# Kernel tuning notes

Hardware: AMD Instinct MI355X
Metric: run time of the kernel (lower is better)

## Reference

```python
import jax, jax.numpy as jnp
import numpy as np

# Static architecture sizes (see shape_source)
B, H, W, NCH = 64, 64, 64, 3
K = 2                     # kernel at every stage
D = 20                    # bond_dim == virtual_dim
OUT = 10                  # output_dim
P1 = (H // K) * (W // K)          # 1024 patches, stage 1
P2 = P1 // (K * K)                # 256 patches, stage 2
P3 = P2 // (K * K)                # 64 patches, stage 3
FP = 2 * K * K                    # feature_dim per stage = 2*ker^2 = 8
FF = 2 * D                        # feature_dim of final MPS = 2*virtual_dim


def _unfold(x, k):
    # torch: x.unfold(2,k,k).unfold(3,k,k).reshape(b, k*k, -1, C)
    b, C, Hh, Ww = x.shape
    v = x.reshape(b, C, Hh // k, k, Ww // k, k).transpose(0, 1, 2, 4, 3, 5)
    return v.reshape(b, k * k, -1, C)   # [b, k^2, P, C] (raw reshape, faithful)


def _batchnorm(y, g, bb, eps=1e-5):
    # BatchNorm1d(C) on [b, C, L], training mode (batch stats), affine
    mu = jnp.mean(y, axis=(0, 2), keepdims=True)
    var = jnp.var(y, axis=(0, 2), keepdims=True)
    return g[None, :, None] * (y - mu) * jax.lax.rsqrt(var + eps) + bb[None, :, None]


def _mps(x, cores, label, alpha, omega):
    # Batched tensor-train contraction over independent per-patch MPS modules.
    # x:     [b, Fraw, P, S]  (S sites per MPS, P independent MPS modules)
    # cores: [P, S, 2*Fraw, D, D], label: [O, D, D], alpha/omega: [D]
    phi = jnp.concatenate([x, 1.0 - x], axis=1)              # [b, F, P, S]
    M = jnp.einsum('bfps,psfij->spbij', phi, cores)          # per-site transfer mats
    def step(c, m):
        return jnp.einsum('pbij,pbjk->pbik', c, m), None
    eye = jnp.broadcast_to(jnp.eye(cores.shape[-1], dtype=x.dtype), M.shape[1:])
    tot, _ = jax.lax.scan(step, eye, M)                      # [P, b, D, D]
    return jnp.einsum('i,pbij,ojk,k->bpo', alpha, tot, label, omega)  # [b, P, O]


def _cores(key, P, S, F):
    # near-identity init; sum_f phi_f = Fraw = F/2, so scale eye by 2/F
    return (jnp.eye(D, dtype=jnp.float32) * (2.0 / F)
            + 0.01 * jax.random.normal(key, (P, S, F, D, D), jnp.float32))


def setup_inputs() -> dict:
    ks = jax.random.split(jax.random.key(0), 12)
    one, zero = jnp.ones((D,), jnp.float32), jnp.zeros
    return {
        'x': jax.random.normal(ks[0], (B, NCH, H, W), jnp.float32),
        'cores1': _cores(ks[1], P1, NCH, FP),
        'label1': 0.1 * jax.random.normal(ks[2], (D, D, D), jnp.float32),
        'alpha1': one, 'omega1': one,
        'g1': jnp.ones((P1,), jnp.float32), 'b1': zero((P1,), jnp.float32),
        'cores2': _cores(ks[3], P2, D, FP),
        'label2': 0.1 * jax.random.normal(ks[4], (D, D, D), jnp.float32),
        'alpha2': one, 'omega2': one,
        'g2': jnp.ones((P2,), jnp.float32), 'b2': zero((P2,), jnp.float32),
        'cores3': _cores(ks[5], P3, D, FP),
        'label3': 0.1 * jax.random.normal(ks[6], (D, D, D), jnp.float32),
        'alpha3': one, 'omega3': one,
        'g3': jnp.ones((P3,), jnp.float32), 'b3': zero((P3,), jnp.float32),
        'coresF': _cores(ks[7], 1, P3, FF),
        'labelF': 0.1 * jax.random.normal(ks[8], (OUT, D, D), jnp.float32),
        'alphaF': one, 'omegaF': one,
    }


def reference(x, cores1, label1, alpha1, omega1, g1, b1,
              cores2, label2, alpha2, omega2, g2, b2,
              cores3, label3, alpha3, omega3, g3, b3,
              coresF, labelF, alphaF, omegaF):
    b = x.shape[0]
    u = _unfold(x, K)                              # [b, 4, P1, 3]
    y = _mps(u, cores1, label1, alpha1, omega1)    # [b, P1, D]
    y = _batchnorm(y, g1, b1).reshape(b, D, H // K, W // K)   # raw view, faithful
    u = _unfold(y, K)                              # [b, 4, P2, D]
    y = _mps(u, cores2, label2, alpha2, omega2)    # [b, P2, D]
    y = _batchnorm(y, g2, b2).reshape(b, D, H // (K * K), W // (K * K))
    u = _unfold(y, K)                              # [b, 4, P3, D]
    y = _mps(u, cores3, label3, alpha3, omega3)    # [b, P3, D]
    y = _batchnorm(y, g3, b3)
    y = jnp.transpose(y, (0, 2, 1))                # [b, D, P3]
    out = _mps(y[:, :, None, :], coresF, labelF, alphaF, omegaF)[:, 0, :]
    return out                                     # [b, OUT]
```

## Files before the change

### kernel.cpp

```cpp
#include <hip/hip_runtime.h>
#include <hip/hip_bf16.h>

typedef __attribute__((ext_vector_type(4))) float f32x4;
typedef __attribute__((ext_vector_type(8))) short s16x8;

static __device__ __forceinline__ short f2bf(float x) {
  __hip_bfloat16 h = __float2bfloat16(x);
  return *reinterpret_cast<short*>(&h);
}

static __device__ __forceinline__ void wave_lgkm0() {
  asm volatile("s_waitcnt lgkmcnt(0)" ::: "memory");
  __builtin_amdgcn_sched_barrier(0);
}

template<int STAGE>
__global__ __launch_bounds__(256)
void k_mps(const float* __restrict__ xsrc, const float* __restrict__ ysrc,
           const float* __restrict__ cores, const float* __restrict__ alpha,
           const float* __restrict__ label, const float* __restrict__ omega,
           const float* __restrict__ gam, const float* __restrict__ bet,
           float* __restrict__ yout) {
  constexpr int S = (STAGE == 1) ? 3 : 20;
  __shared__ __align__(16) float u4[S][64][4];
  __shared__ __align__(16) short Cl[2][32][168];
  __shared__ __align__(16) float vls[64][36];
  __shared__ float Lw_l[400];
  __shared__ float redA[4], redB[4], stats[2];

  const int p = blockIdx.x, t = threadIdx.x;
  const int b = t & 63, q = t >> 6;
  const int m = b & 15, quad = b >> 4;
  const int bl = q * 16 + m;

  const bool two = (t < 144);
  const float* cbase = cores + (size_t)p * S * 3200;

  float p0A[8], p0B[8], p1A[8], p1B[8];
#pragma unroll
  for (int g = 0; g < 8; ++g) p0A[g] = cbase[g * 400 + t];
  if (two) {
#pragma unroll
    for (int g = 0; g < 8; ++g) p0B[g] = cbase[g * 400 + 256 + t];
  }

  for (int e = t; e < 400; e += 256) {
    int o = e / 20, j = e % 20;
    float a = 0.f;
#pragma unroll
    for (int k = 0; k < 20; ++k) a = fmaf(label[o * 400 + j * 20 + k], omega[k], a);
    Lw_l[e] = a;
  }

  {
    int* cz = (int*)&Cl[0][0][0];
    for (int i = t; i < 5376; i += 256) cz[i] = 0;
    for (int i = t; i < 64 * 36; i += 256) {
      int col = i % 36;
      vls[i / 36][col] = (col < 20) ? alpha[col] : 0.f;
    }
  }

  float vr0[4], vr1[4];
  {
    float a0 = alpha[m];
    float a1 = (m < 4) ? alpha[m + 16] : 0.f;
#pragma unroll
    for (int r = 0; r < 4; ++r) { vr0[r] = a0; vr1[r] = a1; }
  }

  for (int k = 0; k < S; ++k) {
    float val;
    if (STAGE == 1) {
      int L = q * 3072 + p * 3 + k;
      int c = L >> 12, r = L & 4095;
      int hh = 2 * (r >> 7) + ((r >> 1) & 1);
      int ww = 2 * ((r >> 2) & 31) + (r & 1);
      val = xsrc[(b * 3 + c) * 4096 + hh * 64 + ww];
    } else if (STAGE == 2) {
      int L = q * 5120 + p * 20 + k;
      int c = L >> 10, r = L & 1023;
      int f = c * 1024 + (2 * (r >> 6) + ((r >> 1) & 1)) * 32
                        + (2 * ((r >> 2) & 15) + (r & 1));
      val = ysrc[f * 64 + b];
    } else {
      int L = q * 1280 + p * 20 + k;
      int c = L >> 8, r = L & 255;
      int f = c * 256 + (2 * (r >> 5) + ((r >> 1) & 1)) * 16
                       + (2 * ((r >> 2) & 7) + (r & 1));
      val = ysrc[f * 64 + b];
    }
    u4[k][b][q] = val;
  }

  auto writeC = [&](int buf, int e, const float* r) {
    int i = e / 20, j = e % 20;
    Cl[buf][j][      i] = f2bf(r[0] - r[4]);
    Cl[buf][j][ 32 + i] = f2bf(r[1] - r[5]);
    Cl[buf][j][ 64 + i] = f2bf(r[2] - r[6]);
    Cl[buf][j][ 96 + i] = f2bf(r[3] - r[7]);
    float cs = r[4] + r[5] + r[6] + r[7];
    if (i == j) cs -= 1.f;
    Cl[buf][j][128 + i] = f2bf(cs);
  };
  auto loadSite = [&](int s, float (&rA)[8], float (&rB)[8]) {
    const float* cs = cbase + (size_t)s * 3200;
#pragma unroll
    for (int g = 0; g < 8; ++g) rA[g] = cs[g * 400 + t];
    if (two) {
#pragma unroll
      for (int g = 0; g < 8; ++g) rB[g] = cs[g * 400 + 256 + t];
    }
  };

  writeC(0, t, p0A);
  if (two) writeC(0, t + 256, p0B);
  if (S > 1) loadSite(1, p0A, p0B);
  if (S > 2) loadSite(2, p1A, p1B);
  __syncthreads();

  auto site_step = [&](int s, int cur, float (&rA)[8], float (&rB)[8]) {
    const float4 uu = *(const float4*)&u4[s][bl][0];
    const float4 va = *(const float4*)&vls[bl][quad * 8];
    const float4 vb = *(const float4*)&vls[bl][quad * 8 + 4];
    const float vv[8] = {va.x, va.y, va.z, va.w, vb.x, vb.y, vb.z, vb.w};
    const float um[5] = {uu.x, uu.y, uu.z, uu.w, 1.f};

    f32x4 acc0, acc1;
#pragma unroll
    for (int r = 0; r < 4; ++r) { acc0[r] = vr0[r]; acc1[r] = vr1[r]; }
#pragma unroll
    for (int kt = 0; kt < 5; ++kt) {
      s16x8 aF;
#pragma unroll
      for (int j2 = 0; j2 < 8; ++j2) aF[j2] = f2bf(vv[j2] * um[kt]);
      const s16x8 bF0 = *(const s16x8*)&Cl[cur][m][kt * 32 + quad * 8];
      const s16x8 bF1 = *(const s16x8*)&Cl[cur][m + 16][kt * 32 + quad * 8];
      acc0 = __builtin_amdgcn_mfma_f32_16x16x32_bf16(aF, bF0, acc0, 0, 0, 0);
      acc1 = __builtin_amdgcn_mfma_f32_16x16x32_bf16(aF, bF1, acc1, 0, 0, 0);
    }

    if (s + 1 < S) {
      writeC(cur ^ 1, t, rA);
      if (two) writeC(cur ^ 1, t + 256, rB);
      if (s + 3 < S) loadSite(s + 3, rA, rB);
    }

#pragma unroll
    for (int r = 0; r < 4; ++r) { vr0[r] = acc0[r]; vr1[r] = acc1[r]; }
#pragma unroll
    for (int r = 0; r < 4; ++r) vls[q * 16 + quad * 4 + r][m] = acc0[r];
    if (m < 4) {
#pragma unroll
      for (int r = 0; r < 4; ++r) vls[q * 16 + quad * 4 + r][m + 16] = acc1[r];
    }
    __syncthreads();
  };

  for (int s = 0; s < S; s += 2) {
    site_step(s, 0, p0A, p0B);
    if (s + 1 < S) site_step(s + 1, 1, p1A, p1B);
  }

  float vf[20];
  {
    const float4 v0 = *(const float4*)&vls[b][0];
    const float4 v1 = *(const float4*)&vls[b][4];
    const float4 v2 = *(const float4*)&vls[b][8];
    const float4 v3 = *(const float4*)&vls[b][12];
    const float4 v4 = *(const float4*)&vls[b][16];
    vf[0]=v0.x; vf[1]=v0.y; vf[2]=v0.z; vf[3]=v0.w;
    vf[4]=v1.x; vf[5]=v1.y; vf[6]=v1.z; vf[7]=v1.w;
    vf[8]=v2.x; vf[9]=v2.y; vf[10]=v2.z; vf[11]=v2.w;
    vf[12]=v3.x; vf[13]=v3.y; vf[14]=v3.z; vf[15]=v3.w;
    vf[16]=v4.x; vf[17]=v4.y; vf[18]=v4.z; vf[19]=v4.w;
  }
  float yo[5];
  float s1 = 0.f, s2 = 0.f;
#pragma unroll
  for (int jj = 0; jj < 5; ++jj) {
    int o = q * 5 + jj;
    float a = 0.f;
#pragma unroll
    for (int j = 0; j < 20; ++j) a = fmaf(vf[j], Lw_l[o * 20 + j], a);
    yo[jj] = a; s1 += a; s2 += a * a;
  }
#pragma unroll
  for (int off = 32; off > 0; off >>= 1) {
    s1 += __shfl_down(s1, off); s2 += __shfl_down(s2, off);
  }
  if (b == 0) { redA[q] = s1; redB[q] = s2; }
  __syncthreads();
  if (t == 0) {
    float S1 = redA[0] + redA[1] + redA[2] + redA[3];
    float S2 = redB[0] + redB[1] + redB[2] + redB[3];
    float mu = S1 * (1.f / 1280.f);
    float var = S2 * (1.f / 1280.f) - mu * mu;
    if (var < 0.f) var = 0.f;
    stats[0] = mu; stats[1] = var;
  }
  __syncthreads();
  float mu = stats[0], var = stats[1];
  float scale = gam[p] / sqrtf(var + 1e-5f);
  float shift = bet[p] - mu * scale;
#pragma unroll
  for (int jj = 0; jj < 5; ++jj) {
    int o = q * 5 + jj;
    yout[(p * 20 + o) * 64 + b] = fmaf(yo[jj], scale, shift);
  }
}

__global__ __launch_bounds__(256)
void k_mbuild(const float* __restrict__ yn3, const float* __restrict__ coresF,
              float* __restrict__ Mmat) {
  __shared__ float ybn[64][20];
  const int s = blockIdx.x >> 2, bq = blockIdx.x & 3;
  const int t = threadIdx.x;
  for (int i = t; i < 1280; i += 256) ybn[i & 63][i >> 6] = yn3[(size_t)s * 1280 + i];
  __syncthreads();
  const float* cfp = coresF + (size_t)s * 16000;
  for (int e = t; e < 400; e += 256) {
    float dlt[20]; float hsum = 0.f;
#pragma unroll
    for (int g = 0; g < 20; ++g) {
      float lo = cfp[g * 400 + e], hi = cfp[(g + 20) * 400 + e];
      dlt[g] = lo - hi; hsum += hi;
    }
    for (int bb = bq * 16; bb < bq * 16 + 16; ++bb) {
      const float4* yb = (const float4*)ybn[bb];
      float yy[20];
      *(float4*)&yy[0]  = yb[0]; *(float4*)&yy[4]  = yb[1];
      *(float4*)&yy[8]  = yb[2]; *(float4*)&yy[12] = yb[3];
      *(float4*)&yy[16] = yb[4];
      float a = hsum;
#pragma unroll
      for (int g = 0; g < 20; ++g) a = fmaf(yy[g], dlt[g], a);
      Mmat[((size_t)s * 64 + bb) * 400 + e] = a;
    }
  }
}

__global__ __launch_bounds__(512)
void k_fin(const float* __restrict__ Mmat, const float* __restrict__ alphaF,
           const float* __restrict__ labelF, const float* __restrict__ omegaF,
           float* __restrict__ out) {
  const int bb = blockIdx.x, t = threadIdx.x;
  const int w = t >> 6, l = t & 63;
  __shared__ float Pw[8][2][400];
  __shared__ float Mw[8][400];
  __shared__ float chunkP[8][400];
  __shared__ float LwF[200];
  __shared__ float va[20];

  if (t < 200) {
    int o = t / 20, j = t % 20;
    float a = 0.f;
#pragma unroll
    for (int k = 0; k < 20; ++k) a = fmaf(labelF[o * 400 + j * 20 + k], omegaF[k], a);
    LwF[t] = a;
  }

  float pre[7];
  {
    const size_t b0 = ((size_t)(w * 8) * 64 + bb) * 400;
#pragma unroll
    for (int it = 0; it < 7; ++it) {
      int e = l + 64 * it;
      pre[it] = (e < 400) ? Mmat[b0 + e] : 0.f;
    }
#pragma unroll
    for (int it = 0; it < 7; ++it) {
      int e = l + 64 * it;
      if (e < 400) Pw[w][0][e] = pre[it];
    }
  }
  int cur = 0;
  for (int ls = 1; ls < 8; ++ls) {
    const size_t mb = ((size_t)(w * 8 + ls) * 64 + bb) * 400;
#pragma unroll
    for (int it = 0; it < 7; ++it) {
      int e = l + 64 * it;
      if (e < 400) pre[it] = Mmat[mb + e];
    }
#pragma unroll
    for (int it = 0; it < 7; ++it) {
      int e = l + 64 * it;
      if (e < 400) Mw[w][e] = pre[it];
    }
    wave_lgkm0();
    if (l < 60) {
      const int j = l % 20, ii = l / 20;
      float mc[20];
#pragma unroll
      for (int k = 0; k < 20; ++k) mc[k] = Mw[w][k * 20 + j];
      for (int i = ii; i < 20; i += 3) {
        float a = 0.f;
#pragma unroll
        for (int k = 0; k < 20; ++k) a = fmaf(Pw[w][cur][i * 20 + k], mc[k], a);
        Pw[w][cur ^ 1][i * 20 + j] = a;
      }
    }
    wave_lgkm0();
    cur ^= 1;
  }
#pragma unroll
  for (int it = 0; it < 7; ++it) {
    int e = l + 64 * it;
    if (e < 400) chunkP[w][e] = Pw[w][cur][e];
  }
  __syncthreads();

  float* T0 = &Mw[0][0];
  float* T1 = &Mw[1][0];
  if (t < 400) T0[t] = chunkP[0][t];
  __syncthreads();
  float* Tc = T0; float* Tn = T1;
  for (int c = 1; c < 8; ++c) {
    if (t < 400) {
      int i = t / 20, j = t - (t / 20) * 20;
      float a = 0.f;
#pragma unroll
      for (int k = 0; k < 20; ++k) a = fmaf(Tc[i * 20 + k], chunkP[c][k * 20 + j], a);
      Tn[t] = a;
    }
    __syncthreads();
    float* tmp = Tc; Tc = Tn; Tn = tmp;
  }
  if (t < 20) {
    float a = 0.f;
#pragma unroll
    for (int i = 0; i < 20; ++i) a = fmaf(alphaF[i], Tc[i * 20 + t], a);
    va[t] = a;
  }
  __syncthreads();
  if (t < 10) {
    float a = 0.f;
#pragma unroll
    for (int j = 0; j < 20; ++j) a = fmaf(va[j], LwF[t * 20 + j], a);
    out[bb * 10 + t] = a;
  }
}

extern "C" void kernel_launch(void* const* d_in, const int* in_sizes, int n_in,
                              void* d_out, int out_size, void* d_ws, size_t ws_size,
                              hipStream_t stream) {
  const float* x      = (const float*)d_in[0];
  const float* cores1 = (const float*)d_in[1];
  const float* label1 = (const float*)d_in[2];
  const float* alpha1 = (const float*)d_in[3];
  const float* omega1 = (const float*)d_in[4];
  const float* g1     = (const float*)d_in[5];
  const float* b1     = (const float*)d_in[6];
  const float* cores2 = (const float*)d_in[7];
  const float* label2 = (const float*)d_in[8];
  const float* alpha2 = (const float*)d_in[9];
  const float* omega2 = (const float*)d_in[10];
  const float* g2     = (const float*)d_in[11];
  const float* b2     = (const float*)d_in[12];
  const float* cores3 = (const float*)d_in[13];
  const float* label3 = (const float*)d_in[14];
  const float* alpha3 = (const float*)d_in[15];
  const float* omega3 = (const float*)d_in[16];
  const float* g3     = (const float*)d_in[17];
  const float* b3     = (const float*)d_in[18];
  const float* coresF = (const float*)d_in[19];
  const float* labelF = (const float*)d_in[20];
  const float* alphaF = (const float*)d_in[21];
  const float* omegaF = (const float*)d_in[22];

  float* ws   = (float*)d_ws;
  float* yn1  = ws;
  float* yn2  = yn1 + 1310720;
  float* yn3  = yn2 + 327680;
  float* Mmat = yn3 + 81920;
  float* out  = (float*)d_out;

  k_mps<1><<<1024, 256, 0, stream>>>(x, nullptr, cores1, alpha1, label1, omega1, g1, b1, yn1);
  k_mps<2><<<256, 256, 0, stream>>>(nullptr, yn1, cores2, alpha2, label2, omega2, g2, b2, yn2);
  k_mps<3><<<64, 256, 0, stream>>>(nullptr, yn2, cores3, alpha3, label3, omega3, g3, b3, yn3);
  k_mbuild<<<256, 256, 0, stream>>>(yn3, coresF, Mmat);
  k_fin<<<64, 512, 0, stream>>>(Mmat, alphaF, labelF, omegaF, out);
}
```

Before: 254.2 us.

## Fuse final-MPS matrix build into stage 3 and split chain product across blocks

Stage 3 now writes its batch-normalised output to shared memory and builds the final MPS transfer matrices directly, which removes the separate k_mbuild launch and the yn3 round trip. The final chain product, previously 64 blocks of 512 threads, is split into 512 single-wave blocks that each multiply 8 matrices with register prefetch and float4 LDS reads, followed by a small kernel that combines the 8 chunk products per batch element. This raises parallelism in the sequential tail in exchange for an extra launch and a global chunk buffer. The fused stage-3 matrix build runs on only 64 blocks, each looping over all 64 batch entries, so it may itself become slower.

```diff
diff --git a/kernel.cpp b/kernel.cpp
--- a/kernel.cpp
+++ b/kernel.cpp
@@ -20,7 +20,8 @@
            const float* __restrict__ cores, const float* __restrict__ alpha,
            const float* __restrict__ label, const float* __restrict__ omega,
            const float* __restrict__ gam, const float* __restrict__ bet,
-           float* __restrict__ yout) {
+           float* __restrict__ yout, const float* __restrict__ coresF,
+           float* __restrict__ Mmat) {
   constexpr int S = (STAGE == 1) ? 3 : 20;
   __shared__ __align__(16) float u4[S][64][4];
   __shared__ __align__(16) short Cl[2][32][168];
@@ -203,101 +204,105 @@
   float mu = stats[0], var = stats[1];
   float scale = gam[p] / sqrtf(var + 1e-5f);
   float shift = bet[p] - mu * scale;
-#pragma unroll
-  for (int jj = 0; jj < 5; ++jj) {
-    int o = q * 5 + jj;
-    yout[(p * 20 + o) * 64 + b] = fmaf(yo[jj], scale, shift);
-  }
-}
-
-__global__ __launch_bounds__(256)
-void k_mbuild(const float* __restrict__ yn3, const float* __restrict__ coresF,
-              float* __restrict__ Mmat) {
-  __shared__ float ybn[64][20];
-  const int s = blockIdx.x >> 2, bq = blockIdx.x & 3;
-  const int t = threadIdx.x;
-  for (int i = t; i < 1280; i += 256) ybn[i & 63][i >> 6] = yn3[(size_t)s * 1280 + i];
-  __syncthreads();
-  const float* cfp = coresF + (size_t)s * 16000;
-  for (int e = t; e < 400; e += 256) {
-    float dlt[20]; float hsum = 0.f;
-#pragma unroll
-    for (int g = 0; g < 20; ++g) {
-      float lo = cfp[g * 400 + e], hi = cfp[(g + 20) * 400 + e];
-      dlt[g] = lo - hi; hsum += hi;
-    }
-    for (int bb = bq * 16; bb < bq * 16 + 16; ++bb) {
-      const float4* yb = (const float4*)ybn[bb];
-      float yy[20];
-      *(float4*)&yy[0]  = yb[0]; *(float4*)&yy[4]  = yb[1];
-      *(float4*)&yy[8]  = yb[2]; *(float4*)&yy[12] = yb[3];
-      *(float4*)&yy[16] = yb[4];
-      float a = hsum;
-#pragma unroll
-      for (int g = 0; g < 20; ++g) a = fmaf(yy[g], dlt[g], a);
-      Mmat[((size_t)s * 64 + bb) * 400 + e] = a;
-    }
-  }
-}
-
-__global__ __launch_bounds__(512)
-void k_fin(const float* __restrict__ Mmat, const float* __restrict__ alphaF,
-           const float* __restrict__ labelF, const float* __restrict__ omegaF,
-           float* __restrict__ out) {
-  const int bb = blockIdx.x, t = threadIdx.x;
-  const int w = t >> 6, l = t & 63;
-  __shared__ float Pw[8][2][400];
-  __shared__ float Mw[8][400];
-  __shared__ float chunkP[8][400];
-  __shared__ float LwF[200];
-  __shared__ float va[20];
-
-  if (t < 200) {
-    int o = t / 20, j = t % 20;
-    float a = 0.f;
-#pragma unroll
-    for (int k = 0; k < 20; ++k) a = fmaf(labelF[o * 400 + j * 20 + k], omegaF[k], a);
-    LwF[t] = a;
-  }
-
+
+  if constexpr (STAGE != 3) {
+#pragma unroll
+    for (int jj = 0; jj < 5; ++jj) {
+      int o = q * 5 + jj;
+      yout[(p * 20 + o) * 64 + b] = fmaf(yo[jj], scale, shift);
+    }
+  } else {
+#pragma unroll
+    for (int jj = 0; jj < 5; ++jj) {
+      int o = q * 5 + jj;
+      vls[b][o] = fmaf(yo[jj], scale, shift);
+    }
+    __syncthreads();
+    const float* cfp = coresF + (size_t)p * 16000;
+    for (int e = t; e < 400; e += 256) {
+      float dlt[20]; float hsum = 0.f;
+#pragma unroll
+      for (int g = 0; g < 20; ++g) {
+        float lo = cfp[g * 400 + e], hi = cfp[(g + 20) * 400 + e];
+        dlt[g] = lo - hi; hsum += hi;
+      }
+      for (int bb = 0; bb < 64; ++bb) {
+        const float4* yb = (const float4*)&vls[bb][0];
+        float yy[20];
+        *(float4*)&yy[0]  = yb[0]; *(float4*)&yy[4]  = yb[1];
+        *(float4*)&yy[8]  = yb[2]; *(float4*)&yy[12] = yb[3];
+        *(float4*)&yy[16] = yb[4];
+        float a = hsum;
+#pragma unroll
+        for (int g = 0; g < 20; ++g) a = fmaf(yy[g], dlt[g], a);
+        Mmat[((size_t)p * 64 + bb) * 400 + e] = a;
+      }
+    }
+  }
+}
+
+__global__ __launch_bounds__(64)
+void k_finA(const float* __restrict__ Mmat, float* __restrict__ chunkPg) {
+  const int bid = blockIdx.x;
+  const int bb = bid & 63, c = bid >> 6;
+  const int l = threadIdx.x;
+  __shared__ float Pb[2][400];
+  __shared__ float Mb[400];
+
+  const size_t base0 = ((size_t)(c * 8) * 64 + bb) * 400;
+#pragma unroll
+  for (int it = 0; it < 7; ++it) {
+    int e = l + 64 * it;
+    if (e < 400) Pb[0][e] = Mmat[base0 + e];
+  }
   float pre[7];
   {
-    const size_t b0 = ((size_t)(w * 8) * 64 + bb) * 400;
+    const size_t base1 = ((size_t)(c * 8 + 1) * 64 + bb) * 400;
 #pragma unroll
     for (int it = 0; it < 7; ++it) {
       int e = l + 64 * it;
-      pre[it] = (e < 400) ? Mmat[b0 + e] : 0.f;
-    }
+      pre[it] = (e < 400) ? Mmat[base1 + e] : 0.f;
+    }
+  }
+  int cur = 0;
+  for (int ls = 1; ls < 8; ++ls) {
 #pragma unroll
     for (int it = 0; it < 7; ++it) {
       int e = l + 64 * it;
-      if (e < 400) Pw[w][0][e] = pre[it];
-    }
-  }
-  int cur = 0;
-  for (int ls = 1; ls < 8; ++ls) {
-    const size_t mb = ((size_t)(w * 8 + ls) * 64 + bb) * 400;
-#pragma unroll
-    for (int it = 0; it < 7; ++it) {
-      int e = l + 64 * it;
-      if (e < 400) pre[it] = Mmat[mb + e];
-    }
-#pragma unroll
-    for (int it = 0; it < 7; ++it) {
-      int e = l + 64 * it;
-      if (e < 400) Mw[w][e] = pre[it];
+      if (e < 400) Mb[e] = pre[it];
+    }
+    if (ls + 1 < 8) {
+      const size_t mb2 = ((size_t)(c * 8 + ls + 1) * 64 + bb) * 400;
+#pragma unroll
+      for (int it = 0; it < 7; ++it) {
+        int e = l + 64 * it;
+        if (e < 400) pre[it] = Mmat[mb2 + e];
+      }
     }
     wave_lgkm0();
     if (l < 60) {
       const int j = l % 20, ii = l / 20;
       float mc[20];
 #pragma unroll
-      for (int k = 0; k < 20; ++k) mc[k] = Mw[w][k * 20 + j];
+      for (int k = 0; k < 20; ++k) mc[k] = Mb[k * 20 + j];
       for (int i = ii; i < 20; i += 3) {
+        const float4 p0 = *(const float4*)&Pb[cur][i * 20 + 0];
+        const float4 p1 = *(const float4*)&Pb[cur][i * 20 + 4];
+        const float4 p2 = *(const float4*)&Pb[cur][i * 20 + 8];
+        const float4 p3 = *(const float4*)&Pb[cur][i * 20 + 12];
+        const float4 p4 = *(const float4*)&Pb[cur][i * 20 + 16];
         float a = 0.f;
-#pragma unroll
-        for (int k = 0; k < 20; ++k) a = fmaf(Pw[w][cur][i * 20 + k], mc[k], a);
-        Pw[w][cur ^ 1][i * 20 + j] = a;
+        a = fmaf(p0.x, mc[0],  a); a = fmaf(p0.y, mc[1],  a);
+        a = fmaf(p0.z, mc[2],  a); a = fmaf(p0.w, mc[3],  a);
+        a = fmaf(p1.x, mc[4],  a); a = fmaf(p1.y, mc[5],  a);
+        a = fmaf(p1.z, mc[6],  a); a = fmaf(p1.w, mc[7],  a);
+        a = fmaf(p2.x, mc[8],  a); a = fmaf(p2.y, mc[9],  a);
+        a = fmaf(p2.z, mc[10], a); a = fmaf(p2.w, mc[11], a);
+        a = fmaf(p3.x, mc[12], a); a = fmaf(p3.y, mc[13], a);
+        a = fmaf(p3.z, mc[14], a); a = fmaf(p3.w, mc[15], a);
+        a = fmaf(p4.x, mc[16], a); a = fmaf(p4.y, mc[17], a);
+        a = fmaf(p4.z, mc[18], a); a = fmaf(p4.w, mc[19], a);
+        Pb[cur ^ 1][i * 20 + j] = a;
       }
     }
     wave_lgkm0();
@@ -306,30 +311,46 @@
 #pragma unroll
   for (int it = 0; it < 7; ++it) {
     int e = l + 64 * it;
-    if (e < 400) chunkP[w][e] = Pw[w][cur][e];
-  }
-  __syncthreads();
-
-  float* T0 = &Mw[0][0];
-  float* T1 = &Mw[1][0];
-  if (t < 400) T0[t] = chunkP[0][t];
-  __syncthreads();
-  float* Tc = T0; float* Tn = T1;
+    if (e < 400) chunkPg[((size_t)bb * 8 + c) * 400 + e] = Pb[cur][e];
+  }
+}
+
+__global__ __launch_bounds__(256)
+void k_finB(const float* __restrict__ chunkPg, const float* __restrict__ alphaF,
+            const float* __restrict__ labelF, const float* __restrict__ omegaF,
+            float* __restrict__ out) {
+  const int bb = blockIdx.x, t = threadIdx.x;
+  __shared__ float C[8][400];
+  __shared__ float T[2][400];
+  __shared__ float LwF[200];
+  __shared__ float va[20];
+  for (int i = t; i < 3200; i += 256) C[i / 400][i % 400] = chunkPg[(size_t)bb * 3200 + i];
+  if (t < 200) {
+    int o = t / 20, j = t % 20;
+    float a = 0.f;
+#pragma unroll
+    for (int k = 0; k < 20; ++k) a = fmaf(labelF[o * 400 + j * 20 + k], omegaF[k], a);
+    LwF[t] = a;
+  }
+  __syncthreads();
+  for (int e = t; e < 400; e += 256) T[0][e] = C[0][e];
+  __syncthreads();
+  int cur = 0;
   for (int c = 1; c < 8; ++c) {
-    if (t < 400) {
-      int i = t / 20, j = t - (t / 20) * 20;
+    for (int e = t; e < 400; e += 256) {
+      int i = e / 20, j = e - (e / 20) * 20;
       float a = 0.f;
 #pragma unroll
-      for (int k = 0; k < 20; ++k) a = fmaf(Tc[i * 20 + k], chunkP[c][k * 20 + j], a);
-      Tn[t] = a;
-    }
+      for (int k = 0; k < 20; ++k) a = fmaf(T[cur][i * 20 + k], C[c][k * 20 + j], a);
+      T[cur ^ 1][e] = a;
+    }
+    cur ^= 1;
     __syncthreads();
-    float* tmp = Tc; Tc = Tn; Tn = tmp;
   }
   if (t < 20) {
     float a = 0.f;
 #pragma unroll
-    for (int i = 0; i < 20; ++i) a = fmaf(alphaF[i], Tc[i * 20 + t], a);
+    for (int i = 0; i < 20; ++i) a = fmaf(alphaF[i], T[cur][i * 20 + t], a);
     va[t] = a;
   }
   __syncthreads();
@@ -368,16 +389,19 @@
   const float* alphaF = (const float*)d_in[21];
   const float* omegaF = (const float*)d_in[22];
 
-  float* ws   = (float*)d_ws;
-  float* yn1  = ws;
-  float* yn2  = yn1 + 1310720;
-  float* yn3  = yn2 + 327680;
-  float* Mmat = yn3 + 81920;
-  float* out  = (float*)d_out;
-
-  k_mps<1><<<1024, 256, 0, stream>>>(x, nullptr, cores1, alpha1, label1, omega1, g1, b1, yn1);
-  k_mps<2><<<256, 256, 0, stream>>>(nullptr, yn1, cores2, alpha2, label2, omega2, g2, b2, yn2);
-  k_mps<3><<<64, 256, 0, stream>>>(nullptr, yn2, cores3, alpha3, label3, omega3, g3, b3, yn3);
-  k_mbuild<<<256, 256, 0, stream>>>(yn3, coresF, Mmat);
-  k_fin<<<64, 512, 0, stream>>>(Mmat, alphaF, labelF, omegaF, out);
-}
+  float* ws      = (float*)d_ws;
+  float* yn1     = ws;
+  float* yn2     = yn1 + 1310720;
+  float* Mmat    = yn2 + 327680;
+  float* chunkPg = Mmat + 1638400;
+  float* out     = (float*)d_out;
+
+  k_mps<1><<<1024, 256, 0, stream>>>(x, nullptr, cores1, alpha1, label1, omega1,
+                                     g1, b1, yn1, nullptr, nullptr);
+  k_mps<2><<<256, 256, 0, stream>>>(nullptr, yn1, cores2, alpha2, label2, omega2,
+                                    g2, b2, yn2, nullptr, nullptr);
+  k_mps<3><<<64, 256, 0, stream>>>(nullptr, yn2, cores3, alpha3, label3, omega3,
+                                   g3, b3, nullptr, coresF, Mmat);
+  k_finA<<<512, 64, 0, stream>>>(Mmat, chunkPg);
+  k_finB<<<64, 256, 0, stream>>>(chunkPg, alphaF, labelF, omegaF, out);
+}
```

Result: no change. 256.5 us (+0.9%).

## Stage MPS cores in LDS in phases and use wave-level sync per site

Applied to the files above, without the earlier changes.

Replaces the per-site register prefetch and double-buffered LDS transfer matrices with phases of up to ten sites whose cores are all loaded and converted into LDS at once, followed by a sync-light sequential contraction. Because each wave only reads its own rows of the vector buffer, the per-site block barrier becomes a wave-local lgkmcnt wait, removing many __syncthreads. In exchange, LDS use grows to roughly 100KB for stages 2/3, which may limit occupancy, and global loads are no longer overlapped with the MFMA chain. The unused row slots for the second MFMA now read a duplicated valid row rather than zero padding.

```diff
diff --git a/kernel.cpp b/kernel.cpp
--- a/kernel.cpp
+++ b/kernel.cpp
@@ -21,28 +21,25 @@
            const float* __restrict__ label, const float* __restrict__ omega,
            const float* __restrict__ gam, const float* __restrict__ bet,
            float* __restrict__ yout) {
-  constexpr int S = (STAGE == 1) ? 3 : 20;
-  __shared__ __align__(16) float u4[S][64][4];
-  __shared__ __align__(16) short Cl[2][32][168];
-  __shared__ __align__(16) float vls[64][36];
-  __shared__ float Lw_l[400];
-  __shared__ float redA[4], redB[4], stats[2];
+  constexpr int S  = (STAGE == 1) ? 3 : 20;
+  constexpr int PH = (S < 10) ? S : 10;
+
+  extern __shared__ __align__(16) char smem[];
+  float (*u4)[64][4] = (float (*)[64][4])smem;
+  float (*vls)[36]   = (float (*)[36])(smem + S * 1024);
+  float* Lw_l        = (float*)(smem + S * 1024 + 9216);
+  float* redA        = Lw_l + 400;
+  float* redB        = redA + 4;
+  float* stats       = redB + 4;
+  short (*CS)[20][168] = (short (*)[20][168])(smem + S * 1024 + 9216 + 1600 + 48);
 
   const int p = blockIdx.x, t = threadIdx.x;
   const int b = t & 63, q = t >> 6;
   const int m = b & 15, quad = b >> 4;
   const int bl = q * 16 + m;
-
-  const bool two = (t < 144);
+  const int mrow1 = (m < 4) ? m + 16 : m;
+
   const float* cbase = cores + (size_t)p * S * 3200;
-
-  float p0A[8], p0B[8], p1A[8], p1B[8];
-#pragma unroll
-  for (int g = 0; g < 8; ++g) p0A[g] = cbase[g * 400 + t];
-  if (two) {
-#pragma unroll
-    for (int g = 0; g < 8; ++g) p0B[g] = cbase[g * 400 + 256 + t];
-  }
 
   for (int e = t; e < 400; e += 256) {
     int o = e / 20, j = e % 20;
@@ -53,8 +50,8 @@
   }
 
   {
-    int* cz = (int*)&Cl[0][0][0];
-    for (int i = t; i < 5376; i += 256) cz[i] = 0;
+    int* cz = (int*)&CS[0][0][0];
+    for (int i = t; i < PH * 1680; i += 256) cz[i] = 0;
     for (int i = t; i < 64 * 36; i += 256) {
       int col = i % 36;
       vls[i / 36][col] = (col < 20) ? alpha[col] : 0.f;
@@ -92,74 +89,61 @@
     }
     u4[k][b][q] = val;
   }
-
-  auto writeC = [&](int buf, int e, const float* r) {
-    int i = e / 20, j = e % 20;
-    Cl[buf][j][      i] = f2bf(r[0] - r[4]);
-    Cl[buf][j][ 32 + i] = f2bf(r[1] - r[5]);
-    Cl[buf][j][ 64 + i] = f2bf(r[2] - r[6]);
-    Cl[buf][j][ 96 + i] = f2bf(r[3] - r[7]);
-    float cs = r[4] + r[5] + r[6] + r[7];
-    if (i == j) cs -= 1.f;
-    Cl[buf][j][128 + i] = f2bf(cs);
-  };
-  auto loadSite = [&](int s, float (&rA)[8], float (&rB)[8]) {
-    const float* cs = cbase + (size_t)s * 3200;
-#pragma unroll
-    for (int g = 0; g < 8; ++g) rA[g] = cs[g * 400 + t];
-    if (two) {
-#pragma unroll
-      for (int g = 0; g < 8; ++g) rB[g] = cs[g * 400 + 256 + t];
-    }
-  };
-
-  writeC(0, t, p0A);
-  if (two) writeC(0, t + 256, p0B);
-  if (S > 1) loadSite(1, p0A, p0B);
-  if (S > 2) loadSite(2, p1A, p1B);
-  __syncthreads();
-
-  auto site_step = [&](int s, int cur, float (&rA)[8], float (&rB)[8]) {
-    const float4 uu = *(const float4*)&u4[s][bl][0];
-    const float4 va = *(const float4*)&vls[bl][quad * 8];
-    const float4 vb = *(const float4*)&vls[bl][quad * 8 + 4];
-    const float vv[8] = {va.x, va.y, va.z, va.w, vb.x, vb.y, vb.z, vb.w};
-    const float um[5] = {uu.x, uu.y, uu.z, uu.w, 1.f};
-
-    f32x4 acc0, acc1;
-#pragma unroll
-    for (int r = 0; r < 4; ++r) { acc0[r] = vr0[r]; acc1[r] = vr1[r]; }
-#pragma unroll
-    for (int kt = 0; kt < 5; ++kt) {
-      s16x8 aF;
-#pragma unroll
-      for (int j2 = 0; j2 < 8; ++j2) aF[j2] = f2bf(vv[j2] * um[kt]);
-      const s16x8 bF0 = *(const s16x8*)&Cl[cur][m][kt * 32 + quad * 8];
-      const s16x8 bF1 = *(const s16x8*)&Cl[cur][m + 16][kt * 32 + quad * 8];
-      acc0 = __builtin_amdgcn_mfma_f32_16x16x32_bf16(aF, bF0, acc0, 0, 0, 0);
-      acc1 = __builtin_amdgcn_mfma_f32_16x16x32_bf16(aF, bF1, acc1, 0, 0, 0);
-    }
-
-    if (s + 1 < S) {
-      writeC(cur ^ 1, t, rA);
-      if (two) writeC(cur ^ 1, t + 256, rB);
-      if (s + 3 < S) loadSite(s + 3, rA, rB);
-    }
-
-#pragma unroll
-    for (int r = 0; r < 4; ++r) { vr0[r] = acc0[r]; vr1[r] = acc1[r]; }
-#pragma unroll
-    for (int r = 0; r < 4; ++r) vls[q * 16 + quad * 4 + r][m] = acc0[r];
-    if (m < 4) {
-#pragma unroll
-      for (int r = 0; r < 4; ++r) vls[q * 16 + quad * 4 + r][m + 16] = acc1[r];
+  __syncthreads();
+
+  for (int ph = 0; ph < S; ph += PH) {
+    const int ns = (S - ph < PH) ? (S - ph) : PH;
+
+#pragma unroll 4
+    for (int uidx = t; uidx < ns * 400; uidx += 256) {
+      const int ls = uidx / 400, e = uidx - ls * 400;
+      const float* cs = cbase + (size_t)(ph + ls) * 3200;
+      float r0 = cs[e],        r1 = cs[400 + e],  r2 = cs[800 + e],  r3 = cs[1200 + e];
+      float r4 = cs[1600 + e], r5 = cs[2000 + e], r6 = cs[2400 + e], r7 = cs[2800 + e];
+      const int i = e / 20, j = e - i * 20;
+      short* row = &CS[ls][j][0];
+      row[i]       = f2bf(r0 - r4);
+      row[32 + i]  = f2bf(r1 - r5);
+      row[64 + i]  = f2bf(r2 - r6);
+      row[96 + i]  = f2bf(r3 - r7);
+      float csum = r4 + r5 + r6 + r7;
+      if (i == j) csum -= 1.f;
+      row[128 + i] = f2bf(csum);
     }
     __syncthreads();
-  };
-
-  for (int s = 0; s < S; s += 2) {
-    site_step(s, 0, p0A, p0B);
-    if (s + 1 < S) site_step(s + 1, 1, p1A, p1B);
+
+    for (int ls = 0; ls < ns; ++ls) {
+      const int s = ph + ls;
+      const float4 uu4 = *(const float4*)&u4[s][bl][0];
+      const float4 va4 = *(const float4*)&vls[bl][quad * 8];
+      const float4 vb4 = *(const float4*)&vls[bl][quad * 8 + 4];
+      const float vv[8] = {va4.x, va4.y, va4.z, va4.w, vb4.x, vb4.y, vb4.z, vb4.w};
+      const float um[5] = {uu4.x, uu4.y, uu4.z, uu4.w, 1.f};
+
+      f32x4 acc0, acc1;
+#pragma unroll
+      for (int r = 0; r < 4; ++r) { acc0[r] = vr0[r]; acc1[r] = vr1[r]; }
+#pragma unroll
+      for (int kt = 0; kt < 5; ++kt) {
+        s16x8 aF;
+#pragma unroll
+        for (int j2 = 0; j2 < 8; ++j2) aF[j2] = f2bf(vv[j2] * um[kt]);
+        const s16x8 bF0 = *(const s16x8*)&CS[ls][m][kt * 32 + quad * 8];
+        const s16x8 bF1 = *(const s16x8*)&CS[ls][mrow1][kt * 32 + quad * 8];
+        acc0 = __builtin_amdgcn_mfma_f32_16x16x32_bf16(aF, bF0, acc0, 0, 0, 0);
+        acc1 = __builtin_amdgcn_mfma_f32_16x16x32_bf16(aF, bF1, acc1, 0, 0, 0);
+      }
+#pragma unroll
+      for (int r = 0; r < 4; ++r) { vr0[r] = acc0[r]; vr1[r] = acc1[r]; }
+#pragma unroll
+      for (int r = 0; r < 4; ++r) vls[q * 16 + quad * 4 + r][m] = acc0[r];
+      if (m < 4) {
+#pragma unroll
+        for (int r = 0; r < 4; ++r) vls[q * 16 + quad * 4 + r][m + 16] = acc1[r];
+      }
+      wave_lgkm0();
+    }
+    __syncthreads();
   }
 
   float vf[20];
@@ -375,9 +359,15 @@
   float* Mmat = yn3 + 81920;
   float* out  = (float*)d_out;
 
-  k_mps<1><<<1024, 256, 0, stream>>>(x, nullptr, cores1, alpha1, label1, omega1, g1, b1, yn1);
-  k_mps<2><<<256, 256, 0, stream>>>(nullptr, yn1, cores2, alpha2, label2, omega2, g2, b2, yn2);
-  k_mps<3><<<64, 256, 0, stream>>>(nullptr, yn2, cores3, alpha3, label3, omega3, g3, b3, yn3);
+  const size_t SM1 = 3 * 1024 + 9216 + 1600 + 48 + 3 * 6720;
+  const size_t SM2 = 20 * 1024 + 9216 + 1600 + 48 + 10 * 6720;
+
+  k_mps<1><<<1024, 256, SM1, stream>>>(x, nullptr, cores1, alpha1, label1, omega1,
+                                       g1, b1, yn1);
+  k_mps<2><<<256, 256, SM2, stream>>>(nullptr, yn1, cores2, alpha2, label2, omega2,
+                                      g2, b2, yn2);
+  k_mps<3><<<64, 256, SM2, stream>>>(nullptr, yn2, cores3, alpha3, label3, omega3,
+                                     g3, b3, yn3);
   k_mbuild<<<256, 256, 0, stream>>>(yn3, coresF, Mmat);
   k_fin<<<64, 512, 0, stream>>>(Mmat, alphaF, labelF, omegaF, out);
 }
```

After: 271.8 us. +6.9%, slower.
